# Kernel tuning notes

Hardware: AMD Instinct MI355X
Metric: run time of the kernel (lower is better)

The kernel has to match this reference:

```python
import jax, jax.numpy as jnp
import numpy as np

D = 256; R = 2; K = 32
N = 32768; NE = 1_000_000; NT = 65_536
BETA_MAX = 5.0; GRAD_CLIP = 1.0; STATE_CLIP = 10.0
DAMP = 0.9999  # update_damping=1.0 clamped to 1-1e-4
EPS = 1e-5


def _xavier(key, din, dout, gain=0.5):
    lim = gain * np.sqrt(6.0 / (din + dout))
    return jax.random.uniform(key, (din, dout), jnp.float32, -lim, lim)


def setup_inputs() -> dict:
    key = jax.random.key(0)
    ks = jax.random.split(key, 16)
    inv_sp1 = float(np.log(np.expm1(1.0)))  # inverse softplus of 1.0
    return {
        "X": jax.random.normal(ks[0], (N, D), jnp.float32),
        "c_2": jax.random.randint(ks[1], (NE,), 0, N, jnp.int32),
        "u_2": jax.random.randint(ks[2], (NE,), 0, N, jnp.int32),
        "c_3": jax.random.randint(ks[3], (NT,), 0, N, jnp.int32),
        "u_3": jax.random.randint(ks[4], (NT,), 0, N, jnp.int32),
        "v_3": jax.random.randint(ks[5], (NT,), 0, N, jnp.int32),
        "t_tau": jax.random.randint(ks[6], (NT,), 0, 2, jnp.int32),
        "step_size": jnp.float32(0.1),
        "ln_gamma": jnp.ones((D,), jnp.float32),
        "ln_beta": jnp.zeros((D,), jnp.float32),
        "W_Q2": _xavier(ks[7], D, D),
        "W_K2": _xavier(ks[8], D, D),
        "W_Q3": _xavier(ks[9], D, R * D),
        "W_K3": _xavier(ks[10], D, R * D),
        "T_tau": 0.02 * jax.random.normal(ks[11], (2, R, D), jnp.float32),
        "W_Qm": _xavier(ks[12], D, D),
        "W_Km": _xavier(ks[13], D, D),
        "B_mem": jax.random.normal(ks[14], (K, D), jnp.float32) / np.sqrt(D),
        "lambda_2": jnp.float32(inv_sp1), "lambda_3": jnp.float32(inv_sp1), "lambda_m": jnp.float32(inv_sp1),
        "beta_2": jnp.float32(inv_sp1), "beta_3": jnp.float32(inv_sp1), "beta_m": jnp.float32(inv_sp1),
    }


def _seg_lse(s, seg, n):
    # logsumexp of s grouped by seg; empty segments contribute 0
    m = jax.ops.segment_max(s, seg, num_segments=n)
    m0 = jnp.where(jnp.isfinite(m), m, 0.0)
    e = jax.ops.segment_sum(jnp.exp(s - m0[seg]), seg, num_segments=n)
    return jnp.where(e > 0, m0 + jnp.log(jnp.maximum(e, 1e-30)), 0.0)


def _energy(X, ln_gamma, ln_beta, W_Q2, W_K2, W_Q3, W_K3, T_tau, W_Qm, W_Km, B_mem,
            lambda_2, lambda_3, lambda_m, beta_2, beta_3, beta_m,
            c_2, u_2, c_3, u_3, v_3, t_tau):
    mu = X.mean(-1, keepdims=True)
    var = ((X - mu) ** 2).mean(-1, keepdims=True)
    G = (X - mu) * jax.lax.rsqrt(var + EPS) * ln_gamma + ln_beta  # [N,D]
    sp = jax.nn.softplus
    lam2, lam3, lamm = sp(lambda_2), sp(lambda_3), sp(lambda_m)
    b2 = jnp.minimum(sp(beta_2), BETA_MAX)
    b3 = jnp.minimum(sp(beta_3), BETA_MAX)
    bm = jnp.minimum(sp(beta_m), BETA_MAX)
    scale = jnp.float32(1.0 / np.sqrt(D))
    # pairwise (order-2) attention energy over edge list
    Q2, K2 = G @ W_Q2, G @ W_K2
    s2 = b2 * scale * jnp.sum(Q2[c_2] * K2[u_2], axis=-1)  # [NE]
    E2 = -(lam2 / b2) * jnp.sum(_seg_lse(s2, c_2, N))
    # motif (order-3) rank-R energy over triangle list with type embedding T_tau
    Q3 = (G @ W_Q3).reshape(N, R, D)
    K3 = (G @ W_K3).reshape(N, R, D)
    s3 = b3 * scale * jnp.sum(Q3[c_3] * K3[u_3] * K3[v_3] * T_tau[t_tau], axis=(1, 2))  # [NT]
    E3 = -(lam3 / b3) * jnp.sum(_seg_lse(s3, c_3, N))
    # memory-slot energy
    Qm, Km = G @ W_Qm, B_mem @ W_Km  # [N,D],[K,D]
    Sm = bm * scale * (Qm @ Km.T)  # [N,K]
    Em = -(lamm / bm) * jnp.sum(jax.nn.logsumexp(Sm, axis=-1))
    return E2 + E3 + Em


def reference(X, c_2, u_2, c_3, u_3, v_3, t_tau, step_size, ln_gamma, ln_beta,
              W_Q2, W_K2, W_Q3, W_K3, T_tau, W_Qm, W_Km, B_mem,
              lambda_2, lambda_3, lambda_m, beta_2, beta_3, beta_m):
    efn = lambda x: _energy(x, ln_gamma, ln_beta, W_Q2, W_K2, W_Q3, W_K3, T_tau,
                            W_Qm, W_Km, B_mem, lambda_2, lambda_3, lambda_m,
                            beta_2, beta_3, beta_m, c_2, u_2, c_3, u_3, v_3, t_tau)
    E, gX = jax.value_and_grad(efn)(X)
    gn = jnp.maximum(jnp.linalg.norm(gX, axis=-1, keepdims=True), 1e-6)
    gX = gX * jnp.minimum(GRAD_CLIP / gn, 1.0)
    X_next = X - step_size * DAMP * gX
    sn = jnp.maximum(jnp.linalg.norm(X_next, axis=-1, keepdims=True), 1e-6)
    X_next = X_next * jnp.minimum(STATE_CLIP / sn, 1.0)
    return X_next, E
```

## Files before the change

### kernel.cpp

```cpp
#include <hip/hip_runtime.h>
#include <math.h>

#define D_ 256
#define KSLOT 32
#define CAP2 128
#define CAP3C 16
#define CAP3I 32
typedef unsigned short ushort_t;
typedef __attribute__((ext_vector_type(8))) short bf16x8;
typedef __attribute__((ext_vector_type(4))) float f32x4;

__device__ __forceinline__ float softplus_f(float x){
  return (x > 20.0f) ? x : log1pf(expf(x));
}
__device__ __forceinline__ float bflo(unsigned u){ return __uint_as_float(u << 16); }
__device__ __forceinline__ float bfhi(unsigned u){ return __uint_as_float(u & 0xFFFF0000u); }
__device__ __forceinline__ ushort_t f2b(float f){
  unsigned u = __float_as_uint(f);
  unsigned r = u + 0x7FFFu + ((u >> 16) & 1u);
  return (ushort_t)(r >> 16);
}
__device__ __forceinline__ unsigned pack2(float a, float b){
  return (unsigned)f2b(a) | ((unsigned)f2b(b) << 16);
}
__device__ __forceinline__ void unpack16(uint4 a, uint4 b, float* f){
  f[0]=bflo(a.x); f[1]=bfhi(a.x); f[2]=bflo(a.y); f[3]=bfhi(a.y);
  f[4]=bflo(a.z); f[5]=bfhi(a.z); f[6]=bflo(a.w); f[7]=bfhi(a.w);
  f[8]=bflo(b.x); f[9]=bfhi(b.x); f[10]=bflo(b.y); f[11]=bfhi(b.y);
  f[12]=bflo(b.z); f[13]=bfhi(b.z); f[14]=bflo(b.w); f[15]=bfhi(b.w);
}
__device__ __forceinline__ float block_reduce_sum(float v, float* sbuf){
  #pragma unroll
  for (int o = 32; o > 0; o >>= 1) v += __shfl_xor(v, o);
  int t = threadIdx.x, wid = t >> 6, lane = t & 63;
  if (lane == 0) sbuf[wid] = v;
  __syncthreads();
  if (t == 0) sbuf[0] = sbuf[0] + sbuf[1] + sbuf[2] + sbuf[3];
  __syncthreads();
  float r = sbuf[0];
  __syncthreads();
  return r;
}

__global__ __launch_bounds__(256) void zerok(float4* __restrict__ p, size_t n4){
  float4 z; z.x = z.y = z.z = z.w = 0.f;
  for (size_t i = (size_t)blockIdx.x * 256 + threadIdx.x; i < n4; i += (size_t)gridDim.x * 256)
    p[i] = z;
}

__global__ __launch_bounds__(256) void ln_fwd(const float* __restrict__ X, const float* __restrict__ gamma,
    const float* __restrict__ beta, ushort_t* __restrict__ Gb, float* __restrict__ mean, float* __restrict__ rstd)
{
  __shared__ float sbuf[8];
  int n = blockIdx.x, t = threadIdx.x;
  size_t idx = (size_t)n * D_ + t;
  float x = X[idx];
  float mu = block_reduce_sum(x, sbuf) * (1.0f / D_);
  float d = x - mu;
  float var = block_reduce_sum(d * d, sbuf) * (1.0f / D_);
  float rs = rsqrtf(var + 1e-5f);
  Gb[idx] = f2b(d * rs * gamma[t] + beta[t]);
  if (t == 0){ mean[n] = mu; rstd[n] = rs; }
}

__global__ __launch_bounds__(256) void wprep_all(const float* __restrict__ W_Q2, const float* __restrict__ W_K2,
    const float* __restrict__ W_Q3, const float* __restrict__ W_K3, const float* __restrict__ W_Qm,
    ushort_t* __restrict__ WtQm, ushort_t* __restrict__ WtF2, ushort_t* __restrict__ WtF3,
    ushort_t* __restrict__ WbQm, ushort_t* __restrict__ Bt2, ushort_t* __restrict__ Bt3)
{
  int idx = blockIdx.x * 256 + threadIdx.x;
  if (idx < 65536){
    int m = idx >> 8, k = idx & 255;
    WtQm[idx] = f2b(W_Qm[k * 256 + m]);
    return;
  }
  idx -= 65536;
  if (idx < 131072){
    int m = idx >> 8, k = idx & 255;
    WtF2[idx] = f2b(m < 256 ? W_Q2[k * 256 + m] : W_K2[k * 256 + (m - 256)]);
    return;
  }
  idx -= 131072;
  if (idx < 262144){
    int m = idx >> 8, k = idx & 255;
    WtF3[idx] = f2b(m < 512 ? W_Q3[k * 512 + m] : W_K3[k * 512 + (m - 512)]);
    return;
  }
  idx -= 262144;
  if (idx < 65536){ WbQm[idx] = f2b(W_Qm[idx]); return; }
  idx -= 65536;
  if (idx < 131072){
    int d = idx >> 9, k = idx & 511;
    Bt2[idx] = f2b(k < 256 ? W_Q2[d * 256 + k] : W_K2[d * 256 + (k - 256)]);
    return;
  }
  idx -= 131072;
  if (idx < 262144){
    int d = idx >> 10, k = idx & 1023;
    Bt3[idx] = f2b(k < 512 ? W_Q3[d * 512 + k] : W_K3[d * 512 + (k - 512)]);
  }
}

template<int OUT_MODE>
__global__ __launch_bounds__(256) void gemm_bt_mfma(const ushort_t* __restrict__ A,
    const ushort_t* __restrict__ Bt, void* __restrict__ C, int K, int M)
{
  __shared__ __align__(16) ushort_t As[128 * 32];
  __shared__ __align__(16) ushort_t Bs[128 * 32];
  int t = threadIdx.x;
  int wave = t >> 6, lane = t & 63;
  int row0 = blockIdx.y * 128;
  int col0 = blockIdx.x * 128;
  int wrow = (wave & 1) * 64;
  int wcol = (wave >> 1) * 64;
  f32x4 acc[4][4];
  #pragma unroll
  for (int i = 0; i < 4; ++i)
    #pragma unroll
    for (int j = 0; j < 4; ++j)
      acc[i][j] = (f32x4){0.f, 0.f, 0.f, 0.f};
  int srow = wave * 32 + (lane >> 2);
  int skoff = (lane & 3) * 8;
  const ushort_t* Ag0 = A + (size_t)(row0 + srow) * K + skoff;
  const ushort_t* Ag1 = A + (size_t)(row0 + srow + 16) * K + skoff;
  const ushort_t* Bg0 = Bt + (size_t)(col0 + srow) * K + skoff;
  const ushort_t* Bg1 = Bt + (size_t)(col0 + srow + 16) * K + skoff;
  ushort_t* Al0 = As + wave * 1024;
  ushort_t* Al1 = As + wave * 1024 + 512;
  ushort_t* Bl0 = Bs + wave * 1024;
  ushort_t* Bl1 = Bs + wave * 1024 + 512;
  int lrow = lane & 15, lk = (lane >> 4) * 8;
  for (int k0 = 0; k0 < K; k0 += 32){
    __syncthreads();
    __builtin_amdgcn_global_load_lds((const __attribute__((address_space(1))) void*)(Ag0 + k0),
                                     (__attribute__((address_space(3))) void*)Al0, 16, 0, 0);
    __builtin_amdgcn_global_load_lds((const __attribute__((address_space(1))) void*)(Ag1 + k0),
                                     (__attribute__((address_space(3))) void*)Al1, 16, 0, 0);
    __builtin_amdgcn_global_load_lds((const __attribute__((address_space(1))) void*)(Bg0 + k0),
                                     (__attribute__((address_space(3))) void*)Bl0, 16, 0, 0);
    __builtin_amdgcn_global_load_lds((const __attribute__((address_space(1))) void*)(Bg1 + k0),
                                     (__attribute__((address_space(3))) void*)Bl1, 16, 0, 0);
    __syncthreads();
    bf16x8 af[4], bf_[4];
    #pragma unroll
    for (int i = 0; i < 4; ++i)
      af[i] = *(const bf16x8*)(As + (wrow + i * 16 + lrow) * 32 + lk);
    #pragma unroll
    for (int j = 0; j < 4; ++j)
      bf_[j] = *(const bf16x8*)(Bs + (wcol + j * 16 + lrow) * 32 + lk);
    #pragma unroll
    for (int i = 0; i < 4; ++i)
      #pragma unroll
      for (int j = 0; j < 4; ++j)
        acc[i][j] = __builtin_amdgcn_mfma_f32_16x16x32_bf16(af[i], bf_[j], acc[i][j], 0, 0, 0);
  }
  int rbase = row0 + wrow + (lane >> 4) * 4;
  int cbase = col0 + wcol + (lane & 15);
  #pragma unroll
  for (int i = 0; i < 4; ++i){
    #pragma unroll
    for (int r = 0; r < 4; ++r){
      size_t rowoff = (size_t)(rbase + i * 16 + r) * M;
      #pragma unroll
      for (int j = 0; j < 4; ++j){
        int col = cbase + j * 16;
        float v = acc[i][j][r];
        if (OUT_MODE == 0)      ((float*)C)[rowoff + col] = v;
        else if (OUT_MODE == 1) ((float*)C)[rowoff + col] += v;
        else                    ((ushort_t*)C)[rowoff + col] = f2b(v);
      }
    }
  }
}

__global__ __launch_bounds__(256) void km_kernel(const float* __restrict__ Bm, const float* __restrict__ W,
    ushort_t* __restrict__ Kmb)
{
  __shared__ float sb[D_];
  int k = blockIdx.x, t = threadIdx.x;
  if (k < KSLOT){
    sb[t] = Bm[(size_t)k * D_ + t];
    __syncthreads();
    float acc = 0.f;
    for (int d = 0; d < D_; ++d) acc += sb[d] * W[(size_t)d * D_ + t];
    Kmb[(size_t)k * D_ + t] = f2b(acc);
  } else {
    Kmb[(size_t)k * D_ + t] = 0;
  }
}

__global__ __launch_bounds__(256) void softmax32(const float* __restrict__ Sm, ushort_t* __restrict__ Pb,
    float* __restrict__ lseM, const float* __restrict__ bmp, const float* __restrict__ lmp)
{
  int t = threadIdx.x;
  int r = blockIdx.x * 8 + (t >> 5);
  int lane = t & 31;
  float bs = fminf(softplus_f(*bmp), 5.0f) * 0.0625f;
  float coef = -softplus_f(*lmp) * 0.0625f;
  float s = Sm[(size_t)r * 128 + lane] * bs;
  float m = s;
  #pragma unroll
  for (int o = 16; o > 0; o >>= 1) m = fmaxf(m, __shfl_xor(m, o, 32));
  float e = expf(s - m);
  float se = e;
  #pragma unroll
  for (int o = 16; o > 0; o >>= 1) se += __shfl_xor(se, o, 32);
  ushort_t* dst = Pb + (size_t)r * 128 + lane;
  dst[0] = f2b(coef * e / se);
  dst[32] = 0; dst[64] = 0; dst[96] = 0;
  if (lane == 0) lseM[r] = m + logf(se);
}

__global__ __launch_bounds__(256) void scatter2(const int* __restrict__ c2, const int* __restrict__ u2,
    int* __restrict__ cntC, int* __restrict__ cntU, int* __restrict__ adjc, int* __restrict__ adju, int NE_)
{
  int e = blockIdx.x * 256 + threadIdx.x;
  if (e >= NE_) return;
  int c = c2[e], u = u2[e];
  int pc = atomicAdd(cntC + c, 1);
  int gs = (c << 7) + pc;
  bool okc = (pc < CAP2);
  if (okc) adjc[gs] = u;
  int pu = atomicAdd(cntU + u, 1);
  if (pu < CAP2 && okc) adju[(u << 7) + pu] = gs;
}

__global__ __launch_bounds__(256) void scatter3(const int* __restrict__ c3, const int* __restrict__ u3,
    const int* __restrict__ v3, const int* __restrict__ tt, int* __restrict__ cnt3C, int* __restrict__ cnt3I,
    unsigned* __restrict__ adj3c, uint2* __restrict__ adj3i, int NT_)
{
  int e = blockIdx.x * 256 + threadIdx.x;
  if (e >= NT_) return;
  int c = c3[e], u = u3[e], v = v3[e], tau = tt[e];
  int pc = atomicAdd(cnt3C + c, 1);
  if (pc >= CAP3C) return;
  int cslot = (c << 4) + pc;
  adj3c[cslot] = (unsigned)u | ((unsigned)v << 15) | ((unsigned)tau << 30);
  int pu = atomicAdd(cnt3I + u, 1);
  if (pu < CAP3I){
    uint2 eu; eu.x = (unsigned)c | ((unsigned)tau << 15) | ((unsigned)v << 16); eu.y = (unsigned)cslot;
    adj3i[(u << 5) + pu] = eu;
  }
  int pv = atomicAdd(cnt3I + v, 1);
  if (pv < CAP3I){
    uint2 ev; ev.x = (unsigned)c | ((unsigned)tau << 15) | ((unsigned)u << 16); ev.y = (unsigned)cslot;
    adj3i[(v << 5) + pv] = ev;
  }
}

__global__ __launch_bounds__(256) void e2_rowc(const ushort_t* __restrict__ QK2, const int* __restrict__ cntC,
    const int* __restrict__ adjc, ushort_t* __restrict__ dstage, float* __restrict__ s2e,
    float2* __restrict__ ml2, const float* __restrict__ b2p, const float* __restrict__ l2p)
{
  int wave = threadIdx.x >> 6, lane = threadIdx.x & 63;
  int r = blockIdx.x * 4 + wave;
  int quarter = lane >> 4, sub = lane & 15;
  float b2s = fminf(softplus_f(*b2p), 5.0f) * 0.0625f;
  float lam2 = softplus_f(*l2p);
  int start = r << 7;
  int deg = cntC[r]; if (deg > CAP2) deg = CAP2;
  int end = start + deg;
  const ushort_t* qrow = QK2 + (size_t)r * 512 + sub * 16;
  float qf[16];
  unpack16(*(const uint4*)qrow, *(const uint4*)(qrow + 8), qf);
  float m = -1e30f, l = 0.f;
  float a[16] = {};
  for (int p = start + quarter; p < end; p += 4){
    int u = adjc[p];
    const ushort_t* krow = QK2 + (size_t)u * 512 + 256 + sub * 16;
    float kf[16];
    unpack16(*(const uint4*)krow, *(const uint4*)(krow + 8), kf);
    float d = 0.f;
    #pragma unroll
    for (int j = 0; j < 16; ++j) d += qf[j] * kf[j];
    d += __shfl_xor(d, 1); d += __shfl_xor(d, 2); d += __shfl_xor(d, 4); d += __shfl_xor(d, 8);
    float s = d * b2s;
    if (sub == 0) s2e[p] = s;
    float mn = fmaxf(m, s);
    float sc = expf(m - mn);
    float pt = expf(s - mn);
    l = l * sc + pt;
    #pragma unroll
    for (int j = 0; j < 16; ++j) a[j] = a[j] * sc + pt * kf[j];
    m = mn;
  }
  float M = fmaxf(m, __shfl_xor(m, 16)); M = fmaxf(M, __shfl_xor(M, 32));
  float scq = expf(m - M);
  float L = l * scq;
  L += __shfl_xor(L, 16); L += __shfl_xor(L, 32);
  #pragma unroll
  for (int j = 0; j < 16; ++j){
    float x = a[j] * scq;
    x += __shfl_xor(x, 16); x += __shfl_xor(x, 32);
    a[j] = x;
  }
  float linv = 0.f, coef = 0.f;
  if (deg > 0){ linv = 1.0f / L; coef = -lam2 * 0.0625f * linv; }
  if (lane == 0){
    float2 ml; ml.x = M; ml.y = linv;
    ml2[r] = ml;
  }
  if (quarter == 0){
    ushort_t* dst = dstage + (size_t)r * 512 + sub * 16;
    uint4 p0, p1;
    p0.x = pack2(coef*a[0], coef*a[1]);   p0.y = pack2(coef*a[2], coef*a[3]);
    p0.z = pack2(coef*a[4], coef*a[5]);   p0.w = pack2(coef*a[6], coef*a[7]);
    p1.x = pack2(coef*a[8], coef*a[9]);   p1.y = pack2(coef*a[10], coef*a[11]);
    p1.z = pack2(coef*a[12], coef*a[13]); p1.w = pack2(coef*a[14], coef*a[15]);
    *(uint4*)dst = p0; *(uint4*)(dst + 8) = p1;
  }
}

__global__ __launch_bounds__(256) void e2_rowu(const ushort_t* __restrict__ QK2, const int* __restrict__ cntU,
    const int* __restrict__ adju, const float* __restrict__ s2e, const float2* __restrict__ ml2,
    ushort_t* __restrict__ dstage, const float* __restrict__ l2p)
{
  int wave = threadIdx.x >> 6, lane = threadIdx.x & 63;
  int r = blockIdx.x * 4 + wave;
  int quarter = lane >> 4, sub = lane & 15;
  float lam2 = softplus_f(*l2p);
  int start = r << 7;
  int deg = cntU[r]; if (deg > CAP2) deg = CAP2;
  int end = start + deg;
  float a[16] = {};
  for (int p = start + quarter; p < end; p += 4){
    int gs = adju[p];
    int c = gs >> 7;
    float2 ml = ml2[c];
    float pe = expf(s2e[gs] - ml.x) * ml.y;
    const ushort_t* qrow = QK2 + (size_t)c * 512 + sub * 16;
    float qf[16];
    unpack16(*(const uint4*)qrow, *(const uint4*)(qrow + 8), qf);
    #pragma unroll
    for (int j = 0; j < 16; ++j) a[j] += pe * qf[j];
  }
  #pragma unroll
  for (int j = 0; j < 16; ++j){
    float x = a[j];
    x += __shfl_xor(x, 16); x += __shfl_xor(x, 32);
    a[j] = x;
  }
  float coef = -lam2 * 0.0625f;
  if (quarter == 0){
    ushort_t* dst = dstage + (size_t)r * 512 + 256 + sub * 16;
    uint4 p0, p1;
    p0.x = pack2(coef*a[0], coef*a[1]);   p0.y = pack2(coef*a[2], coef*a[3]);
    p0.z = pack2(coef*a[4], coef*a[5]);   p0.w = pack2(coef*a[6], coef*a[7]);
    p1.x = pack2(coef*a[8], coef*a[9]);   p1.y = pack2(coef*a[10], coef*a[11]);
    p1.z = pack2(coef*a[12], coef*a[13]); p1.w = pack2(coef*a[14], coef*a[15]);
    *(uint4*)dst = p0; *(uint4*)(dst + 8) = p1;
  }
}

__global__ __launch_bounds__(256) void e3_rowc(const ushort_t* __restrict__ QK3, const float* __restrict__ Tt,
    const int* __restrict__ cnt3C, const unsigned* __restrict__ adj3c, ushort_t* __restrict__ dstage,
    float* __restrict__ s3c, float2* __restrict__ ml3, const float* __restrict__ b3p,
    const float* __restrict__ l3p)
{
  __shared__ float sT[1024];
  int wave = threadIdx.x >> 6, lane = threadIdx.x & 63;
  int r = blockIdx.x * 4 + wave;
  for (int i = threadIdx.x; i < 1024; i += 256) sT[i] = Tt[i];
  __syncthreads();
  float b3s = fminf(softplus_f(*b3p), 5.0f) * 0.0625f;
  float lam3 = softplus_f(*l3p);
  int start = r << 4;
  int deg = cnt3C[r]; if (deg > CAP3C) deg = CAP3C;
  int end = start + deg;
  uint4 qw = *(const uint4*)(QK3 + (size_t)r * 1024 + lane * 8);
  float q[8] = {bflo(qw.x),bfhi(qw.x),bflo(qw.y),bfhi(qw.y),bflo(qw.z),bfhi(qw.z),bflo(qw.w),bfhi(qw.w)};
  float T0[8], T1[8];
  #pragma unroll
  for (int j = 0; j < 8; ++j){ T0[j] = sT[lane * 8 + j]; T1[j] = sT[512 + lane * 8 + j]; }
  float m = -1e30f, l = 0.f;
  float a[8] = {};
  for (int p = start; p < end; ++p){
    unsigned ent = adj3c[p];
    int u = ent & 32767, v = (ent >> 15) & 32767, tau = (ent >> 30) & 1;
    uint4 bw = *(const uint4*)(QK3 + (size_t)u * 1024 + 512 + lane * 8);
    uint4 cw = *(const uint4*)(QK3 + (size_t)v * 1024 + 512 + lane * 8);
    float kb[8] = {bflo(bw.x),bfhi(bw.x),bflo(bw.y),bfhi(bw.y),bflo(bw.z),bfhi(bw.z),bflo(bw.w),bfhi(bw.w)};
    float kc[8] = {bflo(cw.x),bfhi(cw.x),bflo(cw.y),bfhi(cw.y),bflo(cw.z),bfhi(cw.z),bflo(cw.w),bfhi(cw.w)};
    float prod[8];
    float d = 0.f;
    #pragma unroll
    for (int j = 0; j < 8; ++j){
      float tj = tau ? T1[j] : T0[j];
      prod[j] = kb[j] * kc[j] * tj;
      d += q[j] * prod[j];
    }
    #pragma unroll
    for (int o = 32; o > 0; o >>= 1) d += __shfl_xor(d, o);
    float s = d * b3s;
    if (lane == 0) s3c[p] = s;
    float mn = fmaxf(m, s);
    float sc = expf(m - mn);
    float pt = expf(s - mn);
    l = l * sc + pt;
    #pragma unroll
    for (int j = 0; j < 8; ++j) a[j] = a[j]*sc + pt*prod[j];
    m = mn;
  }
  float linv = 0.f, coef = 0.f;
  if (deg > 0){ linv = 1.0f / l; coef = -lam3 * 0.0625f * linv; }
  uint4 o4;
  o4.x = pack2(coef*a[0], coef*a[1]); o4.y = pack2(coef*a[2], coef*a[3]);
  o4.z = pack2(coef*a[4], coef*a[5]); o4.w = pack2(coef*a[6], coef*a[7]);
  *(uint4*)(dstage + (size_t)r * 1024 + lane * 8) = o4;
  if (lane == 0){
    float2 ml; ml.x = m; ml.y = linv;
    ml3[r] = ml;
  }
}

__global__ __launch_bounds__(256) void e3_rowi(const ushort_t* __restrict__ QK3, const float* __restrict__ Tt,
    const int* __restrict__ cnt3I, const uint2* __restrict__ adj3i, const float* __restrict__ s3c,
    const float2* __restrict__ ml3, ushort_t* __restrict__ dstage, const float* __restrict__ l3p)
{
  __shared__ float sT[1024];
  int wave = threadIdx.x >> 6, lane = threadIdx.x & 63;
  int r = blockIdx.x * 4 + wave;
  for (int i = threadIdx.x; i < 1024; i += 256) sT[i] = Tt[i];
  __syncthreads();
  float lam3 = softplus_f(*l3p);
  int start = r << 5;
  int deg = cnt3I[r]; if (deg > CAP3I) deg = CAP3I;
  int end = start + deg;
  float T0[8], T1[8];
  #pragma unroll
  for (int j = 0; j < 8; ++j){ T0[j] = sT[lane * 8 + j]; T1[j] = sT[512 + lane * 8 + j]; }
  float a[8] = {};
  for (int p = start; p < end; ++p){
    uint2 ent = adj3i[p];
    int c = ent.x & 32767, tau = (ent.x >> 15) & 1, other = (ent.x >> 16) & 32767;
    float2 ml = ml3[c];
    float pe = expf(s3c[ent.y] - ml.x) * ml.y;
    uint4 qw = *(const uint4*)(QK3 + (size_t)c * 1024 + lane * 8);
    uint4 ow = *(const uint4*)(QK3 + (size_t)other * 1024 + 512 + lane * 8);
    float q[8] = {bflo(qw.x),bfhi(qw.x),bflo(qw.y),bfhi(qw.y),bflo(qw.z),bfhi(qw.z),bflo(qw.w),bfhi(qw.w)};
    float ko[8] = {bflo(ow.x),bfhi(ow.x),bflo(ow.y),bfhi(ow.y),bflo(ow.z),bfhi(ow.z),bflo(ow.w),bfhi(ow.w)};
    #pragma unroll
    for (int j = 0; j < 8; ++j){
      float tj = tau ? T1[j] : T0[j];
      a[j] += pe * q[j] * ko[j] * tj;
    }
  }
  float coef = -lam3 * 0.0625f;
  uint4 o4;
  o4.x = pack2(coef*a[0], coef*a[1]); o4.y = pack2(coef*a[2], coef*a[3]);
  o4.z = pack2(coef*a[4], coef*a[5]); o4.w = pack2(coef*a[6], coef*a[7]);
  *(uint4*)(dstage + (size_t)r * 1024 + 512 + lane * 8) = o4;
}

__global__ __launch_bounds__(256) void ln_bwd_update(const float* __restrict__ X, const float* __restrict__ dG,
    const float* __restrict__ gamma, const float* __restrict__ mean, const float* __restrict__ rstd,
    const float* __restrict__ step_p, float* __restrict__ out)
{
  __shared__ float sbuf[8];
  int n = blockIdx.x, t = threadIdx.x;
  size_t idx = (size_t)n * D_ + t;
  float x = X[idx];
  float rs = rstd[n];
  float xh = (x - mean[n]) * rs;
  float dxh = dG[idx] * gamma[t];
  float s1 = block_reduce_sum(dxh, sbuf) * (1.0f / D_);
  float s2v = block_reduce_sum(dxh * xh, sbuf) * (1.0f / D_);
  float dx = rs * (dxh - s1 - xh * s2v);
  float gn2 = block_reduce_sum(dx * dx, sbuf);
  float gn = fmaxf(sqrtf(gn2), 1e-6f);
  float gsc = fminf(1.0f / gn, 1.0f);
  float stp = step_p[0] * 0.9999f;
  float xn = x - stp * gsc * dx;
  float sn2 = block_reduce_sum(xn * xn, sbuf);
  float sn = fmaxf(sqrtf(sn2), 1e-6f);
  float ssc = fminf(10.0f / sn, 1.0f);
  out[idx] = xn * ssc;
}

__global__ __launch_bounds__(256) void energy_final(const float2* __restrict__ ml2, const float2* __restrict__ ml3,
    const float* __restrict__ lseM, int n, const float* l2p, const float* l3p, const float* lmp,
    const float* b2p, const float* b3p, const float* bmp, float* __restrict__ outE)
{
  __shared__ float sbuf[8];
  int t = threadIdx.x;
  float a2 = 0.f, a3 = 0.f, am = 0.f;
  for (int i = t; i < n; i += 256){
    float2 v2 = ml2[i];
    if (v2.y > 0.f) a2 += v2.x - logf(v2.y);
    float2 v3 = ml3[i];
    if (v3.y > 0.f) a3 += v3.x - logf(v3.y);
    am += lseM[i];
  }
  float s2 = block_reduce_sum(a2, sbuf);
  float s3 = block_reduce_sum(a3, sbuf);
  float sm = block_reduce_sum(am, sbuf);
  if (t == 0){
    float l2 = softplus_f(*l2p), l3 = softplus_f(*l3p), lm = softplus_f(*lmp);
    float b2 = fminf(softplus_f(*b2p), 5.0f);
    float b3 = fminf(softplus_f(*b3p), 5.0f);
    float bm = fminf(softplus_f(*bmp), 5.0f);
    *outE = -(l2 / b2) * s2 - (l3 / b3) * s3 - (lm / bm) * sm;
  }
}

static inline void zfill(void* p, size_t nElems, hipStream_t stream){
  size_t n4 = nElems / 4;
  int blocks = (int)(((n4 + 255) / 256) < 16384 ? ((n4 + 255) / 256) : 16384);
  if (blocks < 1) blocks = 1;
  zerok<<<blocks, 256, 0, stream>>>((float4*)p, n4);
}

extern "C" void kernel_launch(void* const* d_in, const int* in_sizes, int n_in,
                              void* d_out, int out_size, void* d_ws, size_t ws_size,
                              hipStream_t stream)
{
  const float* X     = (const float*)d_in[0];
  const int*   c2    = (const int*)d_in[1];
  const int*   u2    = (const int*)d_in[2];
  const int*   c3    = (const int*)d_in[3];
  const int*   u3    = (const int*)d_in[4];
  const int*   v3    = (const int*)d_in[5];
  const int*   tt    = (const int*)d_in[6];
  const float* stepp = (const float*)d_in[7];
  const float* gamma = (const float*)d_in[8];
  const float* beta  = (const float*)d_in[9];
  const float* W_Q2  = (const float*)d_in[10];
  const float* W_K2  = (const float*)d_in[11];
  const float* W_Q3  = (const float*)d_in[12];
  const float* W_K3  = (const float*)d_in[13];
  const float* T_tau = (const float*)d_in[14];
  const float* W_Qm  = (const float*)d_in[15];
  const float* W_Km  = (const float*)d_in[16];
  const float* B_mem = (const float*)d_in[17];
  const float* l2p   = (const float*)d_in[18];
  const float* l3p   = (const float*)d_in[19];
  const float* lmp   = (const float*)d_in[20];
  const float* b2p   = (const float*)d_in[21];
  const float* b3p   = (const float*)d_in[22];
  const float* bmp   = (const float*)d_in[23];

  const int N  = in_sizes[0] / D_;
  const int NE = in_sizes[1];
  const int NT = in_sizes[3];
  const size_t ND = (size_t)N * D_;

  char* base = (char*)d_ws;
  size_t off = 0;
  auto alloc = [&](size_t bytes) -> void* {
    void* p = base + off;
    off += (bytes + 255) & ~(size_t)255;
    return p;
  };
  ushort_t* Gb    = (ushort_t*)alloc(ND * 2);
  ushort_t* bufA  = (ushort_t*)alloc(ND * 4 * 2);
  ushort_t* bufB  = (ushort_t*)alloc(ND * 4 * 2);
  int*      zreg  = (int*)     alloc((size_t)4 * N * 4);
  int*      adjc  = (int*)     alloc((size_t)N * CAP2 * 4);
  int*      adju  = (int*)     alloc((size_t)N * CAP2 * 4);
  unsigned* adj3c = (unsigned*)alloc((size_t)N * CAP3C * 4);
  uint2*    adj3i = (uint2*)   alloc((size_t)N * CAP3I * 8);
  float*    s3c   = (float*)   alloc((size_t)N * CAP3C * 4);
  float2*   ml2   = (float2*)  alloc((size_t)N * 8);
  float2*   ml3   = (float2*)  alloc((size_t)N * 8);
  ushort_t* Kmb   = (ushort_t*)alloc((size_t)128 * 256 * 2);
  ushort_t* KWb   = (ushort_t*)alloc((size_t)256 * 128 * 2);
  float*    meanb = (float*)   alloc((size_t)N * 4);
  float*    rstdb = (float*)   alloc((size_t)N * 4);
  float*    lseM  = (float*)   alloc((size_t)N * 4);
  ushort_t* WtQm  = (ushort_t*)alloc(65536 * 2);
  ushort_t* WtF2  = (ushort_t*)alloc(131072 * 2);
  ushort_t* WtF3  = (ushort_t*)alloc(262144 * 2);
  ushort_t* WbQm  = (ushort_t*)alloc(65536 * 2);
  ushort_t* Bt2   = (ushort_t*)alloc(131072 * 2);
  ushort_t* Bt3   = (ushort_t*)alloc(262144 * 2);

  int* cntC  = zreg;
  int* cntU  = zreg + N;
  int* cnt3C = zreg + 2 * N;
  int* cnt3I = zreg + 3 * N;
  float* out = (float*)d_out;
  float*    Sm  = (float*)bufB;
  ushort_t* Pb  = (ushort_t*)(Sm + (size_t)N * 128);
  float*    s2e = (float*)(bufB + ND * 2);

  zfill(zreg, (size_t)4 * N, stream);

  ln_fwd<<<N, 256, 0, stream>>>(X, gamma, beta, Gb, meanb, rstdb);
  wprep_all<<<(917504 + 255) / 256, 256, 0, stream>>>(W_Q2, W_K2, W_Q3, W_K3, W_Qm,
      WtQm, WtF2, WtF3, WbQm, Bt2, Bt3);

  scatter2<<<(NE + 255) / 256, 256, 0, stream>>>(c2, u2, cntC, cntU, adjc, adju, NE);
  scatter3<<<(NT + 255) / 256, 256, 0, stream>>>(c3, u3, v3, tt, cnt3C, cnt3I, adj3c, adj3i, NT);

  dim3 g256(2, N / 128), g512(4, N / 128), g1024(8, N / 128);

  km_kernel<<<128, 256, 0, stream>>>(B_mem, W_Km, Kmb);
  gemm_bt_mfma<2><<<dim3(1, 2), 256, 0, stream>>>(WbQm, Kmb, KWb, 256, 128);
  gemm_bt_mfma<2><<<g256, 256, 0, stream>>>(Gb, WtQm, bufA, D_, D_);
  gemm_bt_mfma<0><<<dim3(1, N / 128), 256, 0, stream>>>(bufA, Kmb, Sm, 256, 128);
  softmax32<<<N / 8, 256, 0, stream>>>(Sm, Pb, lseM, bmp, lmp);
  gemm_bt_mfma<0><<<g256, 256, 0, stream>>>(Pb, KWb, out, 128, D_);

  gemm_bt_mfma<2><<<g512, 256, 0, stream>>>(Gb, WtF2, bufA, D_, 512);
  e2_rowc<<<N / 4, 256, 0, stream>>>(bufA, cntC, adjc, bufB, s2e, ml2, b2p, l2p);
  e2_rowu<<<N / 4, 256, 0, stream>>>(bufA, cntU, adju, s2e, ml2, bufB, l2p);
  gemm_bt_mfma<1><<<g256, 256, 0, stream>>>(bufB, Bt2, out, 512, D_);

  gemm_bt_mfma<2><<<g1024, 256, 0, stream>>>(Gb, WtF3, bufA, D_, 1024);
  e3_rowc<<<N / 4, 256, 0, stream>>>(bufA, T_tau, cnt3C, adj3c, bufB, s3c, ml3, b3p, l3p);
  e3_rowi<<<N / 4, 256, 0, stream>>>(bufA, T_tau, cnt3I, adj3i, s3c, ml3, bufB, l3p);
  gemm_bt_mfma<1><<<g256, 256, 0, stream>>>(bufB, Bt3, out, 1024, D_);

  ln_bwd_update<<<N, 256, 0, stream>>>(X, out, gamma, meanb, rstdb, stepp, out);

  energy_final<<<1, 256, 0, stream>>>(ml2, ml3, lseM, N, l2p, l3p, lmp, b2p, b3p, bmp, out + ND);
}
```

Measured before the change: 951.7 us.

## Replace atomic edge scatter with two-pass radix bucket partition for pair adjacency

Replaces the per-edge global-atomic scatter that builds the pair-edge adjacency lists with a bucketed partition. Each pass runs a block histogram, a scan, a placement step into 256 coarse buckets using shared-memory atomics, and a per-bucket fine pass that builds rows in LDS and writes them out coalesced. This is done once for the center index and once for the neighbor index. The center adjacency is also stored as 16-bit indices to halve its footprint. The aim is to remove contended random global atomics and scattered writes, at the cost of eight small kernel launches, extra passes over the edge list, and a hardcoded assumption that N equals 256×128.

```diff
diff --git a/kernel.cpp b/kernel.cpp
--- a/kernel.cpp
+++ b/kernel.cpp
@@ -6,6 +6,8 @@
 #define CAP2 128
 #define CAP3C 16
 #define CAP3I 32
+#define NBP 256
+#define NBUCK 256
 typedef unsigned short ushort_t;
 typedef __attribute__((ext_vector_type(8))) short bf16x8;
 typedef __attribute__((ext_vector_type(4))) float f32x4;
@@ -211,18 +213,125 @@
   if (lane == 0) lseM[r] = m + logf(se);
 }
 
-__global__ __launch_bounds__(256) void scatter2(const int* __restrict__ c2, const int* __restrict__ u2,
-    int* __restrict__ cntC, int* __restrict__ cntU, int* __restrict__ adjc, int* __restrict__ adju, int NE_)
-{
-  int e = blockIdx.x * 256 + threadIdx.x;
-  if (e >= NE_) return;
-  int c = c2[e], u = u2[e];
-  int pc = atomicAdd(cntC + c, 1);
-  int gs = (c << 7) + pc;
-  bool okc = (pc < CAP2);
-  if (okc) adjc[gs] = u;
-  int pu = atomicAdd(cntU + u, 1);
-  if (pu < CAP2 && okc) adju[(u << 7) + pu] = gs;
+__global__ __launch_bounds__(256) void p2_hist(const unsigned* __restrict__ key, int stride, int NE_, int chunk,
+    unsigned* __restrict__ bh)
+{
+  __shared__ unsigned h[256];
+  int t = threadIdx.x, b = blockIdx.x;
+  h[t] = 0;
+  __syncthreads();
+  int s = b * chunk, e = s + chunk; if (e > NE_) e = NE_;
+  for (int i = s + t; i < e; i += 256)
+    atomicAdd(&h[(key[(size_t)i * stride] >> 7) & 255u], 1u);
+  __syncthreads();
+  bh[b * 256 + t] = h[t];
+}
+
+__global__ __launch_bounds__(256) void p2_scan(unsigned* __restrict__ bh, int nb, unsigned* __restrict__ base)
+{
+  __shared__ unsigned ss[256];
+  int t = threadIdx.x;
+  unsigned tot = 0;
+  for (int b = 0; b < nb; ++b) tot += bh[b * 256 + t];
+  ss[t] = tot;
+  __syncthreads();
+  #pragma unroll
+  for (int o = 1; o < 256; o <<= 1){
+    unsigned v = (t >= o) ? ss[t - o] : 0u;
+    __syncthreads();
+    ss[t] += v;
+    __syncthreads();
+  }
+  unsigned excl = ss[t] - tot;
+  base[t] = excl;
+  if (t == 255) base[256] = ss[t];
+  unsigned run = excl;
+  for (int b = 0; b < nb; ++b){
+    unsigned v = bh[b * 256 + t];
+    bh[b * 256 + t] = run;
+    run += v;
+  }
+}
+
+__global__ __launch_bounds__(256) void p2_place_c(const int* __restrict__ c2, const int* __restrict__ u2,
+    int NE_, int chunk, const unsigned* __restrict__ bh, unsigned* __restrict__ part)
+{
+  __shared__ unsigned cur[256];
+  int t = threadIdx.x, b = blockIdx.x;
+  cur[t] = bh[b * 256 + t];
+  __syncthreads();
+  int s = b * chunk, e = s + chunk; if (e > NE_) e = NE_;
+  for (int i = s + t; i < e; i += 256){
+    unsigned c = (unsigned)c2[i], u = (unsigned)u2[i];
+    unsigned dst = atomicAdd(&cur[c >> 7], 1u);
+    part[dst] = ((c & 127u) << 15) | u;
+  }
+}
+
+__global__ __launch_bounds__(256) void p2_fine_c(const unsigned* __restrict__ part, const unsigned* __restrict__ base,
+    ushort_t* __restrict__ adjc, int* __restrict__ cntC, uint2* __restrict__ pairsU)
+{
+  __shared__ unsigned cnt[128];
+  __shared__ ushort_t stage[128 * 128];
+  int t = threadIdx.x, b = blockIdx.x;
+  if (t < 128) cnt[t] = 0;
+  __syncthreads();
+  int s = (int)base[b], e = (int)base[b + 1];
+  for (int i = s + t; i < e; i += 256){
+    unsigned w = part[i];
+    unsigned r = w >> 15, u = w & 32767u;
+    unsigned slot = atomicAdd(&cnt[r], 1u);
+    uint2 pr;
+    pr.x = u;
+    if (slot < 128u){
+      stage[r * 128 + slot] = (ushort_t)u;
+      pr.y = (((unsigned)b * 128u + r) << 7) | slot;
+    } else {
+      pr.y = 0xFFFFFFFFu;
+    }
+    pairsU[i] = pr;
+  }
+  __syncthreads();
+  if (t < 128) cntC[b * 128 + t] = (int)cnt[t];
+  for (int i = t; i < 16384; i += 256)
+    adjc[(size_t)b * 16384 + i] = stage[i];
+}
+
+__global__ __launch_bounds__(256) void p2_place_u(const uint2* __restrict__ pairs, int NE_, int chunk,
+    const unsigned* __restrict__ bh, uint2* __restrict__ part)
+{
+  __shared__ unsigned cur[256];
+  int t = threadIdx.x, b = blockIdx.x;
+  cur[t] = bh[b * 256 + t];
+  __syncthreads();
+  int s = b * chunk, e = s + chunk; if (e > NE_) e = NE_;
+  for (int i = s + t; i < e; i += 256){
+    uint2 pr = pairs[i];
+    unsigned dst = atomicAdd(&cur[pr.x >> 7], 1u);
+    part[dst] = pr;
+  }
+}
+
+__global__ __launch_bounds__(256) void p2_fine_u(const uint2* __restrict__ part, const unsigned* __restrict__ base,
+    int* __restrict__ adju, int* __restrict__ cntU)
+{
+  __shared__ unsigned cnt[128];
+  __shared__ unsigned stage[128 * 128];
+  int t = threadIdx.x, b = blockIdx.x;
+  if (t < 128) cnt[t] = 0;
+  __syncthreads();
+  int s = (int)base[b], e = (int)base[b + 1];
+  for (int i = s + t; i < e; i += 256){
+    uint2 pr = part[i];
+    if (pr.y == 0xFFFFFFFFu) continue;
+    unsigned r = pr.x & 127u;
+    unsigned slot = atomicAdd(&cnt[r], 1u);
+    if (slot < 128u) stage[r * 128 + slot] = pr.y;
+  }
+  __syncthreads();
+  if (t < 128) cntU[b * 128 + t] = (int)cnt[t];
+  for (int i = t; i < 16384; i += 256)
+    adju[(size_t)b * 16384 + i] = (int)stage[i];
 }
 
 __global__ __launch_bounds__(256) void scatter3(const int* __restrict__ c3, const int* __restrict__ u3,
@@ -249,7 +358,7 @@
 }
 
 __global__ __launch_bounds__(256) void e2_rowc(const ushort_t* __restrict__ QK2, const int* __restrict__ cntC,
-    const int* __restrict__ adjc, ushort_t* __restrict__ dstage, float* __restrict__ s2e,
+    const ushort_t* __restrict__ adjc, ushort_t* __restrict__ dstage, float* __restrict__ s2e,
     float2* __restrict__ ml2, const float* __restrict__ b2p, const float* __restrict__ l2p)
 {
   int wave = threadIdx.x >> 6, lane = threadIdx.x & 63;
@@ -555,7 +664,7 @@
   ushort_t* bufA  = (ushort_t*)alloc(ND * 4 * 2);
   ushort_t* bufB  = (ushort_t*)alloc(ND * 4 * 2);
   int*      zreg  = (int*)     alloc((size_t)4 * N * 4);
-  int*      adjc  = (int*)     alloc((size_t)N * CAP2 * 4);
+  ushort_t* adjc  = (ushort_t*)alloc((size_t)N * CAP2 * 2);
   int*      adju  = (int*)     alloc((size_t)N * CAP2 * 4);
   unsigned* adj3c = (unsigned*)alloc((size_t)N * CAP3C * 4);
   uint2*    adj3i = (uint2*)   alloc((size_t)N * CAP3I * 8);
@@ -583,13 +692,30 @@
   ushort_t* Pb  = (ushort_t*)(Sm + (size_t)N * 128);
   float*    s2e = (float*)(bufB + ND * 2);
 
+  unsigned* partA  = (unsigned*)bufA;
+  uint2*    pairsU = (uint2*)((char*)bufA + ((size_t)8 << 20));
+  unsigned* bhC    = (unsigned*)((char*)bufA + ((size_t)16 << 20));
+  unsigned* bhU    = bhC + NBP * 256;
+  unsigned* baseC  = bhU + NBP * 256;
+  unsigned* baseU  = baseC + 512;
+
   zfill(zreg, (size_t)4 * N, stream);
 
   ln_fwd<<<N, 256, 0, stream>>>(X, gamma, beta, Gb, meanb, rstdb);
   wprep_all<<<(917504 + 255) / 256, 256, 0, stream>>>(W_Q2, W_K2, W_Q3, W_K3, W_Qm,
       WtQm, WtF2, WtF3, WbQm, Bt2, Bt3);
 
-  scatter2<<<(NE + 255) / 256, 256, 0, stream>>>(c2, u2, cntC, cntU, adjc, adju, NE);
+  {
+    int chunk = (NE + NBP - 1) / NBP;
+    p2_hist<<<NBP, 256, 0, stream>>>((const unsigned*)c2, 1, NE, chunk, bhC);
+    p2_scan<<<1, 256, 0, stream>>>(bhC, NBP, baseC);
+    p2_place_c<<<NBP, 256, 0, stream>>>(c2, u2, NE, chunk, bhC, partA);
+    p2_fine_c<<<NBUCK, 256, 0, stream>>>(partA, baseC, adjc, cntC, pairsU);
+    p2_hist<<<NBP, 256, 0, stream>>>((const unsigned*)pairsU, 2, NE, chunk, bhU);
+    p2_scan<<<1, 256, 0, stream>>>(bhU, NBP, baseU);
+    p2_place_u<<<NBP, 256, 0, stream>>>(pairsU, NE, chunk, bhU, (uint2*)partA);
+    p2_fine_u<<<NBUCK, 256, 0, stream>>>((const uint2*)partA, baseU, adju, cntU);
+  }
   scatter3<<<(NT + 255) / 256, 256, 0, stream>>>(c3, u3, v3, tt, cnt3C, cnt3I, adj3c, adj3i, NT);
 
   dim3 g256(2, N / 128), g512(4, N / 128), g1024(8, N / 128);
```

Result: no change. 966.1 us (+1.5%).
